# Performance work log

Hardware: AMD Instinct MI355X
Metric: run time of the kernel (lower is better)

The kernel has to match this reference:

```python
import jax, jax.numpy as jnp
import numpy as np

B, H0, W0, C = 8, 56, 56, 256
KC = VC = C
HID = 4 * C
NH = 8  # ChannelAttention default num_heads


def _ln(x, g, b, eps=1e-5):
    m = x.mean(-1, keepdims=True)
    v = jnp.var(x, axis=-1, keepdims=True)
    return (x - m) * jax.lax.rsqrt(v + eps) * g + b


def _dwconv(x, w, b, H, W):
    # x: [B, N, C] -> depthwise 3x3 on [B, C, H, W]
    Bn, N, Cc = x.shape
    t = x.transpose(0, 2, 1).reshape(Bn, Cc, H, W)
    y = jax.lax.conv_general_dilated(t, w, (1, 1), 'SAME', feature_group_count=Cc,
                                     dimension_numbers=('NCHW', 'OIHW', 'NCHW'))
    y = y + b[None, :, None, None]
    return y.reshape(Bn, Cc, H * W).transpose(0, 2, 1)


def _mixffn(x, H, W, w1, b1, dww, dwb, lg, lb, w2, b2):
    f = x @ w1.T + b1  # fc1(x), reused for the skip (torch computes it twice, same value)
    ax = jax.nn.gelu(_ln(_dwconv(f, dww, dwb, H, W) + f, lg, lb), approximate=False)
    return ax @ w2.T + b2


def _eff_attn(xn, kw, kb, qw, qb, vw, vb, rw, rb):
    # 1x1 convs == per-pixel linear; head_count=1
    k = jax.nn.softmax(xn @ kw.T + kb, axis=1)  # softmax over spatial N
    q = jax.nn.softmax(xn @ qw.T + qb, axis=2)  # softmax over key channels
    v = xn @ vw.T + vb
    ctx = jnp.einsum('bnk,bnv->bkv', k, v)      # [B, KC, VC]
    att = jnp.einsum('bkv,bnk->bnv', ctx, q)    # [B, N, VC]
    return att @ rw.T + rb


def _chan_attn(xn, temp, qkv_w, pw, pb):
    Bn, N, Cc = xn.shape
    d = Cc // NH
    qkv = (xn @ qkv_w.T).reshape(Bn, N, 3, NH, d).transpose(2, 0, 3, 4, 1)  # [3,B,h,d,N]
    q, k, v = qkv[0], qkv[1], qkv[2]
    q = q / jnp.maximum(jnp.linalg.norm(q, axis=-1, keepdims=True), 1e-12)
    k = k / jnp.maximum(jnp.linalg.norm(k, axis=-1, keepdims=True), 1e-12)
    attn = jax.nn.softmax(jnp.einsum('bhdn,bhen->bhde', q, k) * temp, axis=-1)  # [B,h,d,d]
    out = jnp.einsum('bhde,bhen->bhdn', attn, v).transpose(0, 3, 1, 2).reshape(Bn, N, Cc)
    return out @ pw.T + pb


def _forward(x, ln1g, ln1b, eakw, eakb, eaqw, eaqb, eavw, eavb, earw, earb,
             ln2g, ln2b, m1w1, m1b1, m1dww, m1dwb, m1lg, m1lb, m1w2, m1b2,
             ln3g, ln3b, catemp, caqkvw, capw, capb,
             ln4g, ln4b, m2w1, m2b1, m2dww, m2dwb, m2lg, m2lb, m2w2, m2b2, H, W):
    add1 = x + _eff_attn(_ln(x, ln1g, ln1b), eakw, eakb, eaqw, eaqb, eavw, eavb, earw, earb)
    add2 = add1 + _mixffn(_ln(add1, ln2g, ln2b), H, W, m1w1, m1b1, m1dww, m1dwb, m1lg, m1lb, m1w2, m1b2)
    add3 = add2 + _chan_attn(_ln(add2, ln3g, ln3b), catemp, caqkvw, capw, capb)
    return add3 + _mixffn(_ln(add3, ln4g, ln4b), H, W, m2w1, m2b1, m2dww, m2dwb, m2lg, m2lb, m2w2, m2b2)


def setup_inputs() -> dict:
    key = jax.random.key(0)
    ks = jax.random.split(key, 16)
    s = 0.02
    rn = lambda k, shape: jax.random.normal(k, shape, jnp.float32) * s
    f32 = jnp.float32
    return {
        'x': jax.random.normal(ks[0], (B, H0 * W0, C), f32),
        'H': H0, 'W': W0,
        'ln1g': jnp.ones(C, f32), 'ln1b': jnp.zeros(C, f32),
        'eakw': rn(ks[1], (KC, C)), 'eakb': jnp.zeros(KC, f32),
        'eaqw': rn(ks[2], (KC, C)), 'eaqb': jnp.zeros(KC, f32),
        'eavw': rn(ks[3], (VC, C)), 'eavb': jnp.zeros(VC, f32),
        'earw': rn(ks[4], (C, VC)), 'earb': jnp.zeros(C, f32),
        'ln2g': jnp.ones(C, f32), 'ln2b': jnp.zeros(C, f32),
        'm1w1': rn(ks[5], (HID, C)), 'm1b1': jnp.zeros(HID, f32),
        'm1dww': rn(ks[6], (HID, 1, 3, 3)), 'm1dwb': jnp.zeros(HID, f32),
        'm1lg': jnp.ones(HID, f32), 'm1lb': jnp.zeros(HID, f32),
        'm1w2': rn(ks[7], (C, HID)), 'm1b2': jnp.zeros(C, f32),
        'ln3g': jnp.ones(C, f32), 'ln3b': jnp.zeros(C, f32),
        'catemp': jnp.ones((NH, 1, 1), f32),
        'caqkvw': rn(ks[8], (3 * C, C)),
        'capw': rn(ks[9], (C, C)), 'capb': jnp.zeros(C, f32),
        'ln4g': jnp.ones(C, f32), 'ln4b': jnp.zeros(C, f32),
        'm2w1': rn(ks[10], (HID, C)), 'm2b1': jnp.zeros(HID, f32),
        'm2dww': rn(ks[11], (HID, 1, 3, 3)), 'm2dwb': jnp.zeros(HID, f32),
        'm2lg': jnp.ones(HID, f32), 'm2lb': jnp.zeros(HID, f32),
        'm2w2': rn(ks[12], (C, HID)), 'm2b2': jnp.zeros(C, f32),
    }


def reference(x, H, W, ln1g, ln1b, eakw, eakb, eaqw, eaqb, eavw, eavb, earw, earb,
              ln2g, ln2b, m1w1, m1b1, m1dww, m1dwb, m1lg, m1lb, m1w2, m1b2,
              ln3g, ln3b, catemp, caqkvw, capw, capb,
              ln4g, ln4b, m2w1, m2b1, m2dww, m2dwb, m2lg, m2lb, m2w2, m2b2):
    return _forward(x, ln1g, ln1b, eakw, eakb, eaqw, eaqb, eavw, eavb, earw, earb,
                    ln2g, ln2b, m1w1, m1b1, m1dww, m1dwb, m1lg, m1lb, m1w2, m1b2,
                    ln3g, ln3b, catemp, caqkvw, capw, capb,
                    ln4g, ln4b, m2w1, m2b1, m2dww, m2dwb, m2lg, m2lb, m2w2, m2b2, H, W)
```

## Files before the change

kernel.cpp:

```cpp
#include <hip/hip_runtime.h>
#include <hip/hip_bf16.h>

typedef __hip_bfloat16 bf16;
typedef __attribute__((ext_vector_type(8))) short short8;
typedef __attribute__((ext_vector_type(4))) float floatx4;

#define DI __device__ __forceinline__

DI unsigned short bfbits(float f){
    bf16 h = __float2bfloat16(f);
    return *reinterpret_cast<unsigned short*>(&h);
}
DI float bu(unsigned short u){
    union { unsigned int i; float f; } x; x.i = ((unsigned int)u) << 16; return x.f;
}

DI float gelu_exact(float x){
    float z = fabsf(x) * 0.70710678118654752f;
    float t = __builtin_amdgcn_rcpf(fmaf(0.3275911f, z, 1.f));
    float p = t * fmaf(t, fmaf(t, fmaf(t, fmaf(t, 1.061405429f, -1.453152027f),
                    1.421413741f), -0.284496736f), 0.254829592f);
    float e = __expf(-z*z);
    float er = fmaf(-p, e, 1.f);
    er = copysignf(er, x);
    return 0.5f * x * (1.f + er);
}

DI void gload16(const void* g, void* l){
    __builtin_amdgcn_global_load_lds(
        (const __attribute__((address_space(1))) unsigned int*)g,
        (__attribute__((address_space(3))) unsigned int*)l,
        16, 0, 0);
}

static constexpr int BATCH = 8;
static constexpr int HH = 56, WW = 56;
static constexpr int NPOS = HH * WW;
static constexpr int CDIM = 256;
static constexpr int HIDD = 1024;
static constexpr int MTOT = BATCH * NPOS;
static constexpr int NCHUNK = 49;
static constexpr int LP = 40;
static constexpr int TNS = 7;

struct WArgs {
    const float* src[10];
    bf16* dst[10];
    int n[10];
};
__global__ __launch_bounds__(256) void wcvt_kernel(WArgs a){
    int wid = blockIdx.y;
    int i = (blockIdx.x*256 + threadIdx.x) * 8;
    if (i >= a.n[wid]) return;
    const float* s = a.src[wid] + i;
    float4 f0 = *(const float4*)(s);
    float4 f1 = *(const float4*)(s + 4);
    union { uint4 u; unsigned short us[8]; } p;
    p.us[0]=bfbits(f0.x); p.us[1]=bfbits(f0.y); p.us[2]=bfbits(f0.z); p.us[3]=bfbits(f0.w);
    p.us[4]=bfbits(f1.x); p.us[5]=bfbits(f1.y); p.us[6]=bfbits(f1.z); p.us[7]=bfbits(f1.w);
    *(uint4*)(a.dst[wid] + i) = p.u;
}

__global__ __launch_bounds__(256) void wtrans_kernel(const float* __restrict__ w1, const float* __restrict__ w2,
                                                     float* __restrict__ t1, float* __restrict__ t2){
    int i = blockIdx.x*256 + threadIdx.x;
    const float* w = blockIdx.y ? w2 : w1;
    float* t = blockIdx.y ? t2 : t1;
    int tap = i >> 10, c = i & 1023;
    t[i] = w[c*9 + tap];
}

template<typename TC>
__global__ __launch_bounds__(256) void mfma_gemm(
    const bf16* __restrict__ A, const bf16* __restrict__ Bw,
    const float* __restrict__ bias, const float* __restrict__ addend,
    TC* __restrict__ C, int M, int N, int K, int lda,
    long long strA, long long strB, long long strC, long long strAdd)
{
    __shared__ __align__(16) float smemf[8192];
    short* S = (short*)smemf;
    int tid = threadIdx.x;
    int bz = blockIdx.z;
    A  += (long long)bz * strA;
    Bw += (long long)bz * strB;
    C  += (long long)bz * strC;
    if (addend) addend += (long long)bz * strAdd;

    int gx = gridDim.x;
    int nwg = gx * gridDim.y;
    int bidl = blockIdx.y * gx + blockIdx.x;
    int qq = nwg >> 3, rr = nwg & 7;
    int xcd = bidl & 7, ixx = bidl >> 3;
    int tile = (xcd < rr) ? (xcd*(qq+1) + ixx) : (rr*(qq+1) + (xcd-rr)*qq + ixx);
    int n0 = (tile % gx) * 128, m0 = (tile / gx) * 128;

    int w = tid >> 6, lane = tid & 63, lm = lane & 15, quad = lane >> 4;
    int mw = (w >> 1) * 64, nw = (w & 1) * 64;

    int c0 = w*128 + lane, c1 = c0 + 64;
    int ar0 = c0 >> 2, ac0 = (c0 & 3) ^ (ar0 & 3);
    int ar1 = c1 >> 2, ac1 = (c1 & 3) ^ (ar1 & 3);
    int rgA0 = m0 + ar0; if (rgA0 > M-1) rgA0 = M-1;
    int rgA1 = m0 + ar1; if (rgA1 > M-1) rgA1 = M-1;
    short* aL0 = S + (2*w+0)*512;
    short* aL1 = S + (2*w+1)*512;
    short* bL0 = S + 4096 + (2*w+0)*512;
    short* bL1 = S + 4096 + (2*w+1)*512;
    const bf16* Arow0 = A + (long long)rgA0*lda + ac0*8;
    const bf16* Arow1 = A + (long long)rgA1*lda + ac1*8;
    const bf16* Brow0 = Bw + (long long)(n0+ar0)*K + ac0*8;
    const bf16* Brow1 = Bw + (long long)(n0+ar1)*K + ac1*8;

    floatx4 z = {0.f, 0.f, 0.f, 0.f};
    floatx4 acc[4][4];
    #pragma unroll
    for (int mi = 0; mi < 4; mi++)
        #pragma unroll
        for (int ni = 0; ni < 4; ni++) acc[mi][ni] = z;

    int sq = quad ^ (lm & 3);

    auto STAGE = [&](int k0, int poff){
        gload16(Arow0 + k0, aL0 + poff);
        gload16(Arow1 + k0, aL1 + poff);
        gload16(Brow0 + k0, bL0 + poff);
        gload16(Brow1 + k0, bL1 + poff);
    };

    STAGE(0, 0);
    __syncthreads();
    int NS = K >> 5;
    for (int st = 0; st < NS; st++){
        int poff = (st & 1) << 13;
        if (st + 1 < NS) STAGE((st+1)*32, poff ^ 8192);
        short8 af[4], bfr[4];
        #pragma unroll
        for (int mi = 0; mi < 4; mi++)
            af[mi] = *(const short8*)&S[poff + (((mw + mi*16 + lm)<<2) + sq)*8];
        #pragma unroll
        for (int ni = 0; ni < 4; ni++)
            bfr[ni] = *(const short8*)&S[poff + 4096 + (((nw + ni*16 + lm)<<2) + sq)*8];
        #pragma unroll
        for (int mi = 0; mi < 4; mi++)
            #pragma unroll
            for (int ni = 0; ni < 4; ni++)
                acc[mi][ni] = __builtin_amdgcn_mfma_f32_16x16x32_bf16(af[mi], bfr[ni], acc[mi][ni], 0, 0, 0);
        __syncthreads();
    }

    float bvv[4];
    #pragma unroll
    for (int ni = 0; ni < 4; ni++)
        bvv[ni] = bias ? bias[n0 + nw + ni*16 + lm] : 0.f;
    float* esc = smemf + w*1088;
    int rl0 = lane >> 3;
    #pragma unroll
    for (int mi = 0; mi < 4; mi++){
        #pragma unroll
        for (int ni = 0; ni < 4; ni++)
            #pragma unroll
            for (int r = 0; r < 4; r++)
                esc[(quad*4 + r)*68 + ni*16 + lm] = acc[mi][ni][r] + bvv[ni];
        #pragma unroll
        for (int p = 0; p < 2; p++){
            int rloc = p*8 + rl0;
            int rg = m0 + mw + mi*16 + rloc;
            if (rg < M){
                if constexpr (sizeof(TC) == 2){
                    int cl = (lane & 7) * 8;
                    float4 u0 = *(const float4*)&esc[rloc*68 + cl];
                    float4 u1 = *(const float4*)&esc[rloc*68 + cl + 4];
                    if (addend){
                        long long ai = (long long)rg*N + (n0 + nw + cl);
                        float4 a0 = *(const float4*)(addend + ai);
                        float4 a1 = *(const float4*)(addend + ai + 4);
                        u0.x+=a0.x; u0.y+=a0.y; u0.z+=a0.z; u0.w+=a0.w;
                        u1.x+=a1.x; u1.y+=a1.y; u1.z+=a1.z; u1.w+=a1.w;
                    }
                    union { uint4 u; unsigned short us[8]; } pk;
                    pk.us[0]=bfbits(u0.x); pk.us[1]=bfbits(u0.y); pk.us[2]=bfbits(u0.z); pk.us[3]=bfbits(u0.w);
                    pk.us[4]=bfbits(u1.x); pk.us[5]=bfbits(u1.y); pk.us[6]=bfbits(u1.z); pk.us[7]=bfbits(u1.w);
                    *(uint4*)(C + (long long)rg*N + (n0 + nw + cl)) = pk.u;
                } else {
                    int cl4 = (lane & 7) * 4;
                    long long co = (long long)rg*N + (n0 + nw);
                    float4 u0 = *(const float4*)&esc[rloc*68 + cl4];
                    float4 u1 = *(const float4*)&esc[rloc*68 + 32 + cl4];
                    if (addend){
                        float4 a0 = *(const float4*)(addend + co + cl4);
                        float4 a1 = *(const float4*)(addend + co + 32 + cl4);
                        u0.x+=a0.x; u0.y+=a0.y; u0.z+=a0.z; u0.w+=a0.w;
                        u1.x+=a1.x; u1.y+=a1.y; u1.z+=a1.z; u1.w+=a1.w;
                    }
                    *(float4*)(C + co + cl4) = u0;
                    *(float4*)(C + co + 32 + cl4) = u1;
                }
            }
        }
    }
}

__global__ __launch_bounds__(256) void gemm_tn_mfma(const bf16* __restrict__ V, const bf16* __restrict__ Kb,
                                                    float* __restrict__ part){
    __shared__ short As[128*LP];
    __shared__ short Bs[128*LP];
    int tid = threadIdx.x;
    int bz = blockIdx.z;
    int b = bz / TNS, s = bz % TNS;
    const bf16* Vb = V  + (long long)b*NPOS*CDIM;
    const bf16* Kc = Kb + (long long)b*NPOS*CDIM;
    int m0 = blockIdx.y * 128, n0 = blockIdx.x * 128;
    int w = tid >> 6, lane = tid & 63, lm = lane & 15, quad = lane >> 4;
    int mw = (w >> 1) * 64, nw = (w & 1) * 64;

    floatx4 z = {0.f,0.f,0.f,0.f};
    floatx4 acc[4][4];
    #pragma unroll
    for (int mi = 0; mi < 4; mi++)
        #pragma unroll
        for (int ni = 0; ni < 4; ni++) acc[mi][ni] = z;

    int r = tid & 31, cgrp = tid >> 5;

    for (int step = 0; step < 448/32; step++){
        int nb = s*448 + step*32;
        #pragma unroll
        for (int cc = 0; cc < 2; cc++){
            int ch = cgrp*8 + cc*64;
            short8 va = *(const short8*)(Vb + (long long)(nb + r)*CDIM + m0 + ch);
            short8 ka = *(const short8*)(Kc + (long long)(nb + r)*CDIM + n0 + ch);
            #pragma unroll
            for (int i = 0; i < 8; i++){
                As[(ch+i)*LP + r] = va[i];
                Bs[(ch+i)*LP + r] = ka[i];
            }
        }
        __syncthreads();
        short8 af[4], bfr[4];
        #pragma unroll
        for (int mi = 0; mi < 4; mi++)
            af[mi] = *(const short8*)&As[(mw + mi*16 + lm)*LP + quad*8];
        #pragma unroll
        for (int ni = 0; ni < 4; ni++)
            bfr[ni] = *(const short8*)&Bs[(nw + ni*16 + lm)*LP + quad*8];
        #pragma unroll
        for (int mi = 0; mi < 4; mi++)
            #pragma unroll
            for (int ni = 0; ni < 4; ni++)
                acc[mi][ni] = __builtin_amdgcn_mfma_f32_16x16x32_bf16(af[mi], bfr[ni], acc[mi][ni], 0, 0, 0);
        __syncthreads();
    }

    float* pb = part + (long long)bz * CDIM * CDIM;
    #pragma unroll
    for (int ni = 0; ni < 4; ni++){
        int cg = n0 + nw + ni*16 + lm;
        #pragma unroll
        for (int mi = 0; mi < 4; mi++){
            #pragma unroll
            for (int rr = 0; rr < 4; rr++){
                int rg = m0 + mw + mi*16 + quad*4 + rr;
                pb[(long long)rg*CDIM + cg] = acc[mi][ni][rr];
            }
        }
    }
}

__global__ __launch_bounds__(256) void ctx_reduce(const float* __restrict__ part, bf16* __restrict__ ctxb){
    long long idx = (long long)blockIdx.x*256 + threadIdx.x;
    int b = (int)(idx >> 16);
    int rem = (int)(idx & 65535);
    float s = 0.f;
    #pragma unroll
    for (int sp = 0; sp < TNS; sp++)
        s += part[((long long)(b*TNS+sp) << 16) + rem];
    ctxb[idx] = __float2bfloat16(s);
}

DI void st4o(float* p, long long i, float a, float b, float c, float d){
    float4 v = make_float4(a,b,c,d); *(float4*)(p + i) = v;
}
DI void st4o(bf16* p, long long i, float a, float b, float c, float d){
    union { unsigned long long u; unsigned short us[4]; } pk;
    pk.us[0]=bfbits(a); pk.us[1]=bfbits(b); pk.us[2]=bfbits(c); pk.us[3]=bfbits(d);
    *(unsigned long long*)(p + i) = pk.u;
}
template<typename TOUT>
__global__ __launch_bounds__(256) void ln4_kernel(const float* __restrict__ x, const float* __restrict__ g,
                                                  const float* __restrict__ b, TOUT* __restrict__ y){
    int wv = threadIdx.x >> 6, lane = threadIdx.x & 63;
    long long row = (long long)blockIdx.x*4 + wv;
    float4 v = *(const float4*)(x + row*256 + lane*4);
    float s  = v.x + v.y + v.z + v.w;
    float ss = v.x*v.x + v.y*v.y + v.z*v.z + v.w*v.w;
    #pragma unroll
    for (int off = 32; off > 0; off >>= 1){
        s  += __shfl_down(s,  off);
        ss += __shfl_down(ss, off);
    }
    s = __shfl(s, 0); ss = __shfl(ss, 0);
    float mean = s * (1.f/256.f);
    float var  = ss * (1.f/256.f) - mean*mean;
    float inv  = rsqrtf(var + 1e-5f);
    float4 gv = *(const float4*)(g + lane*4);
    float4 bv = *(const float4*)(b + lane*4);
    st4o(y, row*256 + lane*4,
         (v.x-mean)*inv*gv.x + bv.x, (v.y-mean)*inv*gv.y + bv.y,
         (v.z-mean)*inv*gv.z + bv.z, (v.w-mean)*inv*gv.w + bv.w);
}

__global__ __launch_bounds__(256) void colsm_p1(const float* __restrict__ x, float* __restrict__ lmax, float* __restrict__ lsum){
    int b = blockIdx.x / NCHUNK, ch = blockIdx.x % NCHUNK;
    int c = threadIdx.x;
    const float* base = x + ((long long)b*NPOS + ch*64)*512 + c;
    float m = -1e30f;
    for (int r = 0; r < 64; r++) m = fmaxf(m, base[(long long)r*512]);
    float s = 0.f;
    for (int r = 0; r < 64; r++) s += expf(base[(long long)r*512] - m);
    lmax[(long long)blockIdx.x*CDIM + c] = m;
    lsum[(long long)blockIdx.x*CDIM + c] = s;
}
__global__ __launch_bounds__(256) void colsm_p2(const float* __restrict__ lmax, const float* __restrict__ lsum,
                                                float* __restrict__ gmax, float* __restrict__ ginv){
    int b = blockIdx.x; int c = threadIdx.x;
    float g = -1e30f;
    for (int ch = 0; ch < NCHUNK; ch++) g = fmaxf(g, lmax[((long long)b*NCHUNK+ch)*CDIM + c]);
    float s = 0.f;
    for (int ch = 0; ch < NCHUNK; ch++)
        s += lsum[((long long)b*NCHUNK+ch)*CDIM + c] * expf(lmax[((long long)b*NCHUNK+ch)*CDIM + c] - g);
    gmax[b*CDIM + c] = g; ginv[b*CDIM + c] = 1.f / s;
}

__global__ __launch_bounds__(256) void kqsm_kernel(const float* __restrict__ x, const float* __restrict__ bias,
                                                   const float* __restrict__ gmax, const float* __restrict__ ginv,
                                                   bf16* __restrict__ kb, bf16* __restrict__ qb){
    int wv = threadIdx.x >> 6, lane = threadIdx.x & 63;
    long long row = (long long)blockIdx.x*4 + wv;
    int b = blockIdx.x / 784;
    float4 v = *(const float4*)(x + row*512 + 256 + lane*4);
    float4 bb = *(const float4*)(bias + lane*4);
    v.x += bb.x; v.y += bb.y; v.z += bb.z; v.w += bb.w;
    float m = fmaxf(fmaxf(v.x, v.y), fmaxf(v.z, v.w));
    #pragma unroll
    for (int off = 32; off > 0; off >>= 1) m = fmaxf(m, __shfl_down(m, off));
    m = __shfl(m, 0);
    float e0 = expf(v.x - m), e1 = expf(v.y - m), e2 = expf(v.z - m), e3 = expf(v.w - m);
    float s = e0 + e1 + e2 + e3;
    #pragma unroll
    for (int off = 32; off > 0; off >>= 1) s += __shfl_down(s, off);
    s = __shfl(s, 0);
    float inv = 1.f / s;
    st4o(qb, row*256 + lane*4, e0*inv, e1*inv, e2*inv, e3*inv);
    float4 kv = *(const float4*)(x + row*512 + lane*4);
    float4 gm = *(const float4*)(gmax + b*CDIM + lane*4);
    float4 gi = *(const float4*)(ginv + b*CDIM + lane*4);
    st4o(kb, row*256 + lane*4,
         expf(kv.x - gm.x)*gi.x, expf(kv.y - gm.y)*gi.y,
         expf(kv.z - gm.z)*gi.z, expf(kv.w - gm.w)*gi.w);
}

template<bool G>
DI void conv_core(const bf16* __restrict__ fb, const float* __restrict__ wT,
                  int h, int pw, int c0, float* acc0, float* acc1){
    #pragma unroll
    for (int r = 0; r < 3; r++){
        int hy = h - 1 + r;
        bool rv = !G || (hy >= 0 && hy < HH);
        int hyc = G ? min(max(hy, 0), HH-1) : hy;
        float u[4][8];
        #pragma unroll
        for (int c = 0; c < 4; c++){
            int wx = pw - 1 + c;
            bool vv = rv && (!G || (wx >= 0 && wx < WW));
            int wxc = G ? min(max(wx, 0), WW-1) : wx;
            uint4 raw = *(const uint4*)(fb + (long long)(hyc*WW + wxc)*HIDD + c0);
            unsigned short* us = (unsigned short*)&raw;
            #pragma unroll
            for (int i = 0; i < 8; i++){
                float xv = bu(us[i]);
                u[c][i] = (G && !vv) ? 0.f : xv;
            }
        }
        #pragma unroll
        for (int kx = 0; kx < 3; kx++){
            float4 wA = *(const float4*)(wT + (r*3+kx)*1024 + c0);
            float4 wB = *(const float4*)(wT + (r*3+kx)*1024 + c0 + 4);
            float wv[8] = {wA.x,wA.y,wA.z,wA.w,wB.x,wB.y,wB.z,wB.w};
            #pragma unroll
            for (int i = 0; i < 8; i++){
                acc0[i] = fmaf(u[kx][i],   wv[i], acc0[i]);
                acc1[i] = fmaf(u[kx+1][i], wv[i], acc1[i]);
            }
        }
        if (r == 1){
            #pragma unroll
            for (int i = 0; i < 8; i++){ acc0[i] += u[1][i]; acc1[i] += u[2][i]; }
        }
    }
}

__global__ __launch_bounds__(256) void dwconv_ln_gelu_kernel(const bf16* __restrict__ f, const float* __restrict__ wT,
        const float* __restrict__ db, const float* __restrict__ lg, const float* __restrict__ lb, bf16* __restrict__ out){
    __shared__ float rs[4][128], rq[4][128], rfin[8];
    int tid = threadIdx.x;
    int b = blockIdx.x & 7;
    int rem = blockIdx.x >> 3;
    int h = rem / 14, w0 = (rem % 14) * 4;
    const bf16* fb = f + (long long)b * NPOS * HIDD;
    int ph = tid >> 7, ct = tid & 127;
    int c0 = ct * 8;
    int pw = w0 + 2*ph;

    float acc0[8], acc1[8];
    {
        float4 d0 = *(const float4*)(db + c0);
        float4 d1 = *(const float4*)(db + c0 + 4);
        acc0[0]=d0.x; acc0[1]=d0.y; acc0[2]=d0.z; acc0[3]=d0.w;
        acc0[4]=d1.x; acc0[5]=d1.y; acc0[6]=d1.z; acc0[7]=d1.w;
        #pragma unroll
        for (int i = 0; i < 8; i++) acc1[i] = acc0[i];
    }
    bool interior = (h > 0) && (h < HH-1) && (w0 > 0) && (w0 < 52);
    if (interior) conv_core<false>(fb, wT, h, pw, c0, acc0, acc1);
    else          conv_core<true >(fb, wT, h, pw, c0, acc0, acc1);

    {
        float s0=0.f, q0=0.f, s1=0.f, q1=0.f;
        #pragma unroll
        for (int i = 0; i < 8; i++){
            s0 += acc0[i]; q0 += acc0[i]*acc0[i];
            s1 += acc1[i]; q1 += acc1[i]*acc1[i];
        }
        rs[2*ph][ct] = s0; rq[2*ph][ct] = q0;
        rs[2*ph+1][ct] = s1; rq[2*ph+1][ct] = q1;
    }
    __syncthreads();
    {
        int wv = tid >> 6, ln = tid & 63;
        float s = rs[wv][ln] + rs[wv][ln+64];
        float q = rq[wv][ln] + rq[wv][ln+64];
        #pragma unroll
        for (int off = 32; off > 0; off >>= 1){
            s += __shfl_down(s, off);
            q += __shfl_down(q, off);
        }
        if (ln == 0){ rfin[wv] = s; rfin[4+wv] = q; }
    }
    __syncthreads();
    float4 g0 = *(const float4*)(lg + c0), g1 = *(const float4*)(lg + c0 + 4);
    float4 b0 = *(const float4*)(lb + c0), b1 = *(const float4*)(lb + c0 + 4);
    float gg[8] = {g0.x,g0.y,g0.z,g0.w,g1.x,g1.y,g1.z,g1.w};
    float bb[8] = {b0.x,b0.y,b0.z,b0.w,b1.x,b1.y,b1.z,b1.w};
    #pragma unroll
    for (int pp = 0; pp < 2; pp++){
        int g = 2*ph + pp;
        long long n = (long long)b*NPOS + h*WW + (pw + pp);
        float mean = rfin[g] * (1.f/HIDD);
        float var  = rfin[4+g] * (1.f/HIDD) - mean*mean;
        float inv  = rsqrtf(var + 1e-5f);
        const float* ac = pp ? acc1 : acc0;
        union { uint4 u; unsigned short us[8]; } ov;
        #pragma unroll
        for (int i = 0; i < 8; i++){
            float o = (ac[i]-mean)*inv*gg[i] + bb[i];
            ov.us[i] = bfbits(gelu_exact(o));
        }
        *(uint4*)(out + n*HIDD + c0) = ov.u;
    }
}

__global__ __launch_bounds__(256) void ssq_p1(const bf16* __restrict__ qkv, float* __restrict__ lss){
    __shared__ float red[4][64][8];
    int b = blockIdx.x / NCHUNK, ch = blockIdx.x % NCHUNK;
    int tid = threadIdx.x;
    int col = (tid & 63) * 8;
    int rg = tid >> 6;
    float s[8] = {0,0,0,0,0,0,0,0};
    for (int r = rg*16; r < rg*16 + 16; r++){
        long long row = (long long)(b*NPOS + ch*64 + r);
        union { uint4 u; unsigned short us[8]; } v;
        v.u = *(const uint4*)(qkv + row*768 + col);
        #pragma unroll
        for (int i = 0; i < 8; i++){ float f = bu(v.us[i]); s[i] += f*f; }
    }
    #pragma unroll
    for (int i = 0; i < 8; i++) red[rg][tid & 63][i] = s[i];
    __syncthreads();
    if (tid < 64){
        #pragma unroll
        for (int i = 0; i < 8; i++){
            float t = red[0][tid][i] + red[1][tid][i] + red[2][tid][i] + red[3][tid][i];
            lss[(long long)blockIdx.x*512 + tid*8 + i] = t;
        }
    }
}
__global__ __launch_bounds__(256) void ssq_p2(const float* __restrict__ lss, float* __restrict__ invn){
    int b = blockIdx.x; int c = blockIdx.y*256 + threadIdx.x;
    float s = 0.f;
    for (int ch = 0; ch < NCHUNK; ch++) s += lss[((long long)b*NCHUNK+ch)*512 + c];
    invn[b*512 + c] = 1.f / fmaxf(sqrtf(s), 1e-12f);
}

__global__ __launch_bounds__(256) void chanattn_qk_part(const bf16* __restrict__ qkv, const float* __restrict__ invn,
                                                        float* __restrict__ part){
    __shared__ float qs[64][36];
    __shared__ float ks[64][36];
    int bz = blockIdx.x;
    int bh = bz / TNS, s = bz % TNS;
    int b = bh >> 3, hh = bh & 7;
    int tid = threadIdx.x;
    int d = tid >> 3, e0 = (tid & 7) * 4;
    int sr = tid >> 2, sc8 = (tid & 3) * 8;
    float invq[8], invk[8];
    {
        float4 a0 = *(const float4*)(invn + b*512 + hh*32 + sc8);
        float4 a1 = *(const float4*)(invn + b*512 + hh*32 + sc8 + 4);
        float4 b0 = *(const float4*)(invn + b*512 + 256 + hh*32 + sc8);
        float4 b1 = *(const float4*)(invn + b*512 + 256 + hh*32 + sc8 + 4);
        invq[0]=a0.x; invq[1]=a0.y; invq[2]=a0.z; invq[3]=a0.w;
        invq[4]=a1.x; invq[5]=a1.y; invq[6]=a1.z; invq[7]=a1.w;
        invk[0]=b0.x; invk[1]=b0.y; invk[2]=b0.z; invk[3]=b0.w;
        invk[4]=b1.x; invk[5]=b1.y; invk[6]=b1.z; invk[7]=b1.w;
    }
    float acc[4] = {0.f,0.f,0.f,0.f};
    for (int it = 0; it < 7; it++){
        int n0 = s*448 + it*64;
        {
            long long rowb = (long long)(b*NPOS + n0 + sr) * 768;
            union { uint4 u; unsigned short us[8]; } qv, kv;
            qv.u = *(const uint4*)(qkv + rowb + hh*32 + sc8);
            kv.u = *(const uint4*)(qkv + rowb + 256 + hh*32 + sc8);
            #pragma unroll
            for (int i = 0; i < 8; i++){
                qs[sr][sc8+i] = bu(qv.us[i]) * invq[i];
                ks[sr][sc8+i] = bu(kv.us[i]) * invk[i];
            }
        }
        __syncthreads();
        #pragma unroll 4
        for (int r = 0; r < 64; r++){
            float qv = qs[r][d];
            #pragma unroll
            for (int j = 0; j < 4; j++) acc[j] += qv * ks[r][e0+j];
        }
        __syncthreads();
    }
    #pragma unroll
    for (int j = 0; j < 4; j++)
        part[(long long)bz*1024 + d*32 + e0 + j] = acc[j];
}
__global__ __launch_bounds__(256) void chanattn_qk_fin(const float* __restrict__ part, const float* __restrict__ temp,
                                                       float* __restrict__ attn){
    __shared__ float att_s[32][33];
    int bh = blockIdx.x;
    int hh = bh & 7;
    int tid = threadIdx.x;
    int d = tid >> 3, e0 = (tid & 7) * 4;
    float t = temp[hh];
    #pragma unroll
    for (int j = 0; j < 4; j++){
        float s = 0.f;
        for (int sp = 0; sp < TNS; sp++)
            s += part[((long long)bh*TNS + sp)*1024 + d*32 + e0 + j];
        att_s[d][e0+j] = s * t;
    }
    __syncthreads();
    if (tid < 32){
        float m = -1e30f;
        for (int e = 0; e < 32; e++) m = fmaxf(m, att_s[tid][e]);
        float s = 0.f;
        for (int e = 0; e < 32; e++){ float ev = expf(att_s[tid][e] - m); att_s[tid][e] = ev; s += ev; }
        float inv = 1.f / s;
        for (int e = 0; e < 32; e++) att_s[tid][e] *= inv;
    }
    __syncthreads();
    #pragma unroll
    for (int j = 0; j < 4; j++)
        attn[(long long)bh*1024 + d*32 + e0 + j] = att_s[d][e0+j];
}

__global__ __launch_bounds__(256) void wcomb_kernel(const float* __restrict__ capw, const float* __restrict__ attn,
                                                    bf16* __restrict__ Wb){
    __shared__ float at_s[8192];
    int b = blockIdx.x, og = blockIdx.y;
    int tid = threadIdx.x;
    #pragma unroll
    for (int j = 0; j < 8; j++)
        *(float4*)&at_s[tid*32 + j*4] = *(const float4*)(attn + (long long)b*8192 + tid*32 + j*4);
    __syncthreads();
    int o = og*32 + (tid & 31);
    int h = tid >> 5;
    float acc[32];
    #pragma unroll
    for (int e = 0; e < 32; e++) acc[e] = 0.f;
    for (int d = 0; d < 32; d++){
        float w = capw[(long long)o*256 + h*32 + d];
        const float* ar = &at_s[h*1024 + d*32];
        #pragma unroll
        for (int eq = 0; eq < 8; eq++){
            float4 av = *(const float4*)(ar + eq*4);
            acc[eq*4+0] += w*av.x; acc[eq*4+1] += w*av.y;
            acc[eq*4+2] += w*av.z; acc[eq*4+3] += w*av.w;
        }
    }
    bf16* dst = Wb + (long long)b*65536 + (long long)o*256 + h*32;
    #pragma unroll
    for (int eq = 0; eq < 4; eq++){
        union { uint4 u; unsigned short us[8]; } p;
        #pragma unroll
        for (int i = 0; i < 8; i++) p.us[i] = bfbits(acc[eq*8+i]);
        *(uint4*)(dst + eq*8) = p.u;
    }
}

extern "C" void kernel_launch(void* const* d_in, const int* in_sizes, int n_in,
                              void* d_out, int out_size, void* d_ws, size_t ws_size,
                              hipStream_t stream){
    const float* x     = (const float*)d_in[0];
    const float* ln1g  = (const float*)d_in[3];
    const float* ln1b  = (const float*)d_in[4];
    const float* eakw  = (const float*)d_in[5];
    const float* eaqw  = (const float*)d_in[7];
    const float* eaqb  = (const float*)d_in[8];
    const float* eavw  = (const float*)d_in[9];
    const float* eavb  = (const float*)d_in[10];
    const float* earw  = (const float*)d_in[11];
    const float* earb  = (const float*)d_in[12];
    const float* ln2g  = (const float*)d_in[13];
    const float* ln2b  = (const float*)d_in[14];
    const float* m1w1  = (const float*)d_in[15];
    const float* m1b1  = (const float*)d_in[16];
    const float* m1dww = (const float*)d_in[17];
    const float* m1dwb = (const float*)d_in[18];
    const float* m1lg  = (const float*)d_in[19];
    const float* m1lb  = (const float*)d_in[20];
    const float* m1w2  = (const float*)d_in[21];
    const float* m1b2  = (const float*)d_in[22];
    const float* ln3g  = (const float*)d_in[23];
    const float* ln3b  = (const float*)d_in[24];
    const float* catemp= (const float*)d_in[25];
    const float* caqkvw= (const float*)d_in[26];
    const float* capw  = (const float*)d_in[27];
    const float* capb  = (const float*)d_in[28];
    const float* ln4g  = (const float*)d_in[29];
    const float* ln4b  = (const float*)d_in[30];
    const float* m2w1  = (const float*)d_in[31];
    const float* m2b1  = (const float*)d_in[32];
    const float* m2dww = (const float*)d_in[33];
    const float* m2dwb = (const float*)d_in[34];
    const float* m2lg  = (const float*)d_in[35];
    const float* m2lb  = (const float*)d_in[36];
    const float* m2w2  = (const float*)d_in[37];
    const float* m2b2  = (const float*)d_in[38];

    char* base = (char*)d_ws;
    auto alloc = [&](size_t nbytes){ char* p = base; base += (nbytes + 255) & ~(size_t)255; return p; };
    constexpr size_t SZ = (size_t)MTOT*CDIM*4;
    float* R  = (float*)alloc(SZ);
    float* A0 = (float*)alloc(SZ);
    float* A1 = (float*)alloc(SZ);
    float* B0 = (float*)alloc(SZ);
    float* B1 = (float*)alloc(SZ);
    bf16* A0b  = (bf16*)A0;
    bf16* kb   = (bf16*)A0;
    bf16* qb   = A0b + (size_t)MTOT*CDIM;
    bf16* vb   = (bf16*)A1;
    float* KQ  = B0;
    bf16* attb = (bf16*)B0;
    bf16* l2b  = (bf16*)A1;
    bf16* F    = (bf16*)B0;
    bf16* G    = (bf16*)A0;
    bf16* l3b  = (bf16*)B0;
    bf16* Qb   = (bf16*)A0;
    bf16* l4b  = (bf16*)A0;
    bf16* ctxb = (bf16*)alloc((size_t)BATCH*CDIM*CDIM*2);
    float* lmax = (float*)alloc((size_t)BATCH*NCHUNK*CDIM*4);
    float* lsum = (float*)alloc((size_t)BATCH*NCHUNK*CDIM*4);
    float* gmax = (float*)alloc((size_t)BATCH*CDIM*4);
    float* ginv = (float*)alloc((size_t)BATCH*CDIM*4);
    float* lss  = (float*)alloc((size_t)BATCH*NCHUNK*512*4);
    float* invn = (float*)alloc((size_t)BATCH*512*4);
    float* attnb= (float*)alloc((size_t)BATCH*8*32*32*4);
    float* ptn  = (float*)alloc((size_t)BATCH*TNS*CDIM*CDIM*4);
    float* pqk  = (float*)alloc((size_t)BATCH*8*TNS*1024*4);
    bf16* wbuf  = (bf16*)alloc((size_t)1572864*2);
    float* wT1  = (float*)alloc((size_t)9216*4);
    float* wT2  = (float*)alloc((size_t)9216*4);
    bf16* Wcb   = (bf16*)alloc((size_t)BATCH*CDIM*CDIM*2);

    bf16* kqw_b    = wbuf;
    bf16* eavw_b   = wbuf + 131072;
    bf16* earw_b   = wbuf + 196608;
    bf16* m1w1_b   = wbuf + 262144;
    bf16* m1w2_b   = wbuf + 524288;
    bf16* caqkvw_b = wbuf + 786432;
    bf16* m2w1_b   = wbuf + 1048576;
    bf16* m2w2_b   = wbuf + 1310720;

    dim3 blk(256);
    constexpr int MB = MTOT/128;
    long long sA1 = (long long)NPOS*CDIM;
    long long sB1 = (long long)CDIM*CDIM;

    {
        WArgs wa;
        const float* srcs[10] = {eakw, eaqw, eavw, earw, m1w1, m1w2, caqkvw, m2w1, m2w2, m2w2};
        bf16* dsts[10] = {kqw_b, kqw_b + 65536, eavw_b, earw_b, m1w1_b, m1w2_b, caqkvw_b, m2w1_b, m2w2_b, m2w2_b};
        int ns[10] = {65536, 65536, 65536, 65536, 262144, 262144, 196608, 262144, 262144, 0};
        for (int i = 0; i < 10; i++){ wa.src[i]=srcs[i]; wa.dst[i]=dsts[i]; wa.n[i]=ns[i]; }
        wcvt_kernel<<<dim3(128,10), blk, 0, stream>>>(wa);
        wtrans_kernel<<<dim3(36,2), blk, 0, stream>>>(m1dww, m2dww, wT1, wT2);
    }

    ln4_kernel<bf16><<<MTOT/4, blk, 0, stream>>>(x, ln1g, ln1b, A0b);
    mfma_gemm<float><<<dim3(4,MB,1), blk, 0, stream>>>(A0b, kqw_b, nullptr, nullptr, KQ, MTOT, 512, 256, 256, 0,0,0,0);
    mfma_gemm<bf16><<<dim3(2,MB,1), blk, 0, stream>>>(A0b, eavw_b, eavb, nullptr, vb, MTOT, 256, 256, 256, 0,0,0,0);
    colsm_p1<<<BATCH*NCHUNK, blk, 0, stream>>>(KQ, lmax, lsum);
    colsm_p2<<<BATCH, blk, 0, stream>>>(lmax, lsum, gmax, ginv);
    kqsm_kernel<<<MTOT/4, blk, 0, stream>>>(KQ, eaqb, gmax, ginv, kb, qb);
    gemm_tn_mfma<<<dim3(2,2,BATCH*TNS), blk, 0, stream>>>(vb, kb, ptn);
    ctx_reduce<<<(BATCH*65536)/256, blk, 0, stream>>>(ptn, ctxb);
    mfma_gemm<bf16><<<dim3(2,25,BATCH), blk, 0, stream>>>(qb, ctxb, nullptr, nullptr, attb,
            NPOS, 256, 256, 256, sA1, sB1, sA1, 0);
    mfma_gemm<float><<<dim3(2,MB,1), blk, 0, stream>>>(attb, earw_b, earb, x, R, MTOT, 256, 256, 256, 0,0,0,0);

    ln4_kernel<bf16><<<MTOT/4, blk, 0, stream>>>(R, ln2g, ln2b, l2b);
    mfma_gemm<bf16><<<dim3(8,MB,1), blk, 0, stream>>>(l2b, m1w1_b, m1b1, nullptr, F, MTOT, 1024, 256, 256, 0,0,0,0);
    dwconv_ln_gelu_kernel<<<BATCH*HH*14, blk, 0, stream>>>(F, wT1, m1dwb, m1lg, m1lb, G);
    mfma_gemm<float><<<dim3(2,MB,1), blk, 0, stream>>>(G, m1w2_b, m1b2, R, R, MTOT, 256, 1024, 1024, 0,0,0,0);

    ln4_kernel<bf16><<<MTOT/4, blk, 0, stream>>>(R, ln3g, ln3b, l3b);
    mfma_gemm<bf16><<<dim3(6,MB,1), blk, 0, stream>>>(l3b, caqkvw_b, nullptr, nullptr, Qb, MTOT, 768, 256, 256, 0,0,0,0);
    ssq_p1<<<BATCH*NCHUNK, blk, 0, stream>>>(Qb, lss);
    ssq_p2<<<dim3(BATCH,2), blk, 0, stream>>>(lss, invn);
    chanattn_qk_part<<<BATCH*8*TNS, blk, 0, stream>>>(Qb, invn, pqk);
    chanattn_qk_fin<<<BATCH*8, blk, 0, stream>>>(pqk, catemp, attnb);
    wcomb_kernel<<<dim3(BATCH,8), blk, 0, stream>>>(capw, attnb, Wcb);
    mfma_gemm<float><<<dim3(2,25,BATCH), blk, 0, stream>>>(Qb + 512, Wcb, capb, R, R,
            NPOS, 256, 256, 768, (long long)NPOS*768, sB1, sA1, sA1);

    ln4_kernel<bf16><<<MTOT/4, blk, 0, stream>>>(R, ln4g, ln4b, l4b);
    mfma_gemm<bf16><<<dim3(8,MB,1), blk, 0, stream>>>(l4b, m2w1_b, m2b1, nullptr, F, MTOT, 1024, 256, 256, 0,0,0,0);
    dwconv_ln_gelu_kernel<<<BATCH*HH*14, blk, 0, stream>>>(F, wT2, m2dwb, m2lg, m2lb, G);
    mfma_gemm<float><<<dim3(2,MB,1), blk, 0, stream>>>(G, m2w2_b, m2b2, R, (float*)d_out, MTOT, 256, 1024, 1024, 0,0,0,0);
}
```

Before: 551.5 us.

## Fuse residual GEMM with following LayerNorm and widen dwconv to 4 pixels per thread

Adds a gemm_ln kernel that computes a 64-row by full-256-column GEMM tile with bias and residual add, then performs the row LayerNorm in the epilogue and emits the bf16 normalized output. This replaces three separate ln4 kernel launches and their reread of the fp32 residual. The depthwise conv kernel now computes four adjacent pixels per thread to reuse loaded input columns, halving the block count. The trade-offs are fewer, larger GEMM blocks with lower parallelism, and higher register usage in the conv.

```diff
diff --git a/kernel.cpp b/kernel.cpp
--- a/kernel.cpp
+++ b/kernel.cpp
@@ -200,6 +200,173 @@
     }
 }
 
+__global__ __launch_bounds__(256) void gemm_ln(
+    const bf16* __restrict__ A, const bf16* __restrict__ Bw,
+    const float* __restrict__ bias, const float* __restrict__ addend,
+    float* __restrict__ C, bf16* __restrict__ lnout,
+    const float* __restrict__ lg, const float* __restrict__ lb,
+    int M, int K, int lda,
+    long long strA, long long strB, long long strC, long long strAdd, long long strLn)
+{
+    __shared__ __align__(16) float smemf[10240];
+    short* S = (short*)smemf;
+    constexpr int POFF = 10240;
+    int tid = threadIdx.x;
+    int bz = blockIdx.z;
+    A      += (long long)bz * strA;
+    Bw     += (long long)bz * strB;
+    C      += (long long)bz * strC;
+    addend += (long long)bz * strAdd;
+    lnout  += (long long)bz * strLn;
+
+    int nwg = gridDim.y;
+    int bidl = blockIdx.y;
+    int qq = nwg >> 3, rr = nwg & 7;
+    int xcd = bidl & 7, ixx = bidl >> 3;
+    int tile = (xcd < rr) ? (xcd*(qq+1) + ixx) : (rr*(qq+1) + (xcd-rr)*qq + ixx);
+    int m0 = tile * 64;
+
+    int w = tid >> 6, lane = tid & 63, lm = lane & 15, quad = lane >> 4;
+    int nw = w * 64;
+
+    const bf16* gp[5];
+    int lo[5];
+    #pragma unroll
+    for (int t5 = 0; t5 < 5; t5++){
+        int t = w*5 + t5;
+        if (t < 4){
+            int c = t*64 + lane;
+            int row = c >> 2, cg = (c & 3) ^ (row & 3);
+            int rg = m0 + row; if (rg > M-1) rg = M-1;
+            gp[t5] = A + (long long)rg*lda + cg*8;
+            lo[t5] = t*512;
+        } else {
+            int c = (t-4)*64 + lane;
+            int row = c >> 2, cg = (c & 3) ^ (row & 3);
+            gp[t5] = Bw + (long long)row*K + cg*8;
+            lo[t5] = 2048 + (t-4)*512;
+        }
+    }
+
+    floatx4 z = {0.f,0.f,0.f,0.f};
+    floatx4 acc[4][4];
+    #pragma unroll
+    for (int mi = 0; mi < 4; mi++)
+        #pragma unroll
+        for (int ni = 0; ni < 4; ni++) acc[mi][ni] = z;
+
+    int sq = quad ^ (lm & 3);
+
+    auto STAGE = [&](int k0, int poff){
+        #pragma unroll
+        for (int t5 = 0; t5 < 5; t5++)
+            gload16(gp[t5] + k0, S + lo[t5] + poff);
+    };
+
+    STAGE(0, 0);
+    __syncthreads();
+    int NS = K >> 5;
+    for (int st = 0; st < NS; st++){
+        int poff = (st & 1) ? POFF : 0;
+        if (st + 1 < NS) STAGE((st+1)*32, poff ^ POFF);
+        short8 af[4], bfr[4];
+        #pragma unroll
+        for (int mi = 0; mi < 4; mi++)
+            af[mi] = *(const short8*)&S[poff + (((mi*16 + lm)<<2) + sq)*8];
+        #pragma unroll
+        for (int ni = 0; ni < 4; ni++)
+            bfr[ni] = *(const short8*)&S[poff + 2048 + (((nw + ni*16 + lm)<<2) + sq)*8];
+        #pragma unroll
+        for (int mi = 0; mi < 4; mi++)
+            #pragma unroll
+            for (int ni = 0; ni < 4; ni++)
+                acc[mi][ni] = __builtin_amdgcn_mfma_f32_16x16x32_bf16(af[mi], bfr[ni], acc[mi][ni], 0, 0, 0);
+        __syncthreads();
+    }
+
+    float bvv[4];
+    #pragma unroll
+    for (int ni = 0; ni < 4; ni++)
+        bvv[ni] = bias[nw + ni*16 + lm];
+    float* esc  = smemf + w*1088;
+    float* ssum = smemf + 4608;
+    float* ssq  = smemf + 4864;
+    float* mrow = smemf + 5120;
+    float* irow = smemf + 5184;
+    int rl0 = lane >> 3, jo = lane & 7;
+    int cl4 = jo * 4;
+    #pragma unroll
+    for (int mi = 0; mi < 4; mi++){
+        #pragma unroll
+        for (int ni = 0; ni < 4; ni++)
+            #pragma unroll
+            for (int r = 0; r < 4; r++)
+                esc[(quad*4 + r)*68 + ni*16 + lm] = acc[mi][ni][r] + bvv[ni];
+        #pragma unroll
+        for (int p = 0; p < 2; p++){
+            int rloc = p*8 + rl0;
+            int rg = m0 + mi*16 + rloc;
+            long long co = (long long)rg*256 + nw;
+            float4 u0 = *(const float4*)&esc[rloc*68 + cl4];
+            float4 u1 = *(const float4*)&esc[rloc*68 + 32 + cl4];
+            float4 a0 = *(const float4*)(addend + co + cl4);
+            float4 a1 = *(const float4*)(addend + co + 32 + cl4);
+            u0.x+=a0.x; u0.y+=a0.y; u0.z+=a0.z; u0.w+=a0.w;
+            u1.x+=a1.x; u1.y+=a1.y; u1.z+=a1.z; u1.w+=a1.w;
+            *(float4*)(C + co + cl4) = u0;
+            *(float4*)(C + co + 32 + cl4) = u1;
+            float s = u0.x+u0.y+u0.z+u0.w + u1.x+u1.y+u1.z+u1.w;
+            float q = u0.x*u0.x+u0.y*u0.y+u0.z*u0.z+u0.w*u0.w
+                    + u1.x*u1.x+u1.y*u1.y+u1.z*u1.z+u1.w*u1.w;
+            #pragma unroll
+            for (int off = 1; off < 8; off <<= 1){
+                s += __shfl_xor(s, off);
+                q += __shfl_xor(q, off);
+            }
+            if (jo == 0){
+                ssum[w*64 + mi*16 + rloc] = s;
+                ssq [w*64 + mi*16 + rloc] = q;
+            }
+        }
+    }
+    __syncthreads();
+    if (tid < 64){
+        float s = ssum[tid] + ssum[64+tid] + ssum[128+tid] + ssum[192+tid];
+        float q = ssq[tid]  + ssq[64+tid]  + ssq[128+tid]  + ssq[192+tid];
+        float mean = s * (1.f/256.f);
+        float var  = q * (1.f/256.f) - mean*mean;
+        mrow[tid] = mean;
+        irow[tid] = rsqrtf(var + 1e-5f);
+    }
+    __syncthreads();
+    int cl8 = jo * 8;
+    float4 gl0 = *(const float4*)(lg + nw + cl8);
+    float4 gl1 = *(const float4*)(lg + nw + cl8 + 4);
+    float4 bl0 = *(const float4*)(lb + nw + cl8);
+    float4 bl1 = *(const float4*)(lb + nw + cl8 + 4);
+    float gg[8] = {gl0.x,gl0.y,gl0.z,gl0.w,gl1.x,gl1.y,gl1.z,gl1.w};
+    float bbv[8] = {bl0.x,bl0.y,bl0.z,bl0.w,bl1.x,bl1.y,bl1.z,bl1.w};
+    #pragma unroll
+    for (int mi = 0; mi < 4; mi++){
+        #pragma unroll
+        for (int p = 0; p < 2; p++){
+            int rloc = p*8 + rl0;
+            int row64 = mi*16 + rloc;
+            int rg = m0 + row64;
+            float mean = mrow[row64], inv = irow[row64];
+            long long co = (long long)rg*256 + nw + cl8;
+            float4 v0 = *(const float4*)(C + co);
+            float4 v1 = *(const float4*)(C + co + 4);
+            float vv[8] = {v0.x,v0.y,v0.z,v0.w,v1.x,v1.y,v1.z,v1.w};
+            union { uint4 u; unsigned short us[8]; } pk;
+            #pragma unroll
+            for (int i = 0; i < 8; i++)
+                pk.us[i] = bfbits((vv[i]-mean)*inv*gg[i] + bbv[i]);
+            *(uint4*)(lnout + co) = pk.u;
+        }
+    }
+}
+
 __global__ __launch_bounds__(256) void gemm_tn_mfma(const bf16* __restrict__ V, const bf16* __restrict__ Kb,
                                                     float* __restrict__ part){
     __shared__ short As[128*LP];
@@ -360,17 +527,17 @@
 }
 
 template<bool G>
-DI void conv_core(const bf16* __restrict__ fb, const float* __restrict__ wT,
-                  int h, int pw, int c0, float* acc0, float* acc1){
+DI void conv_core4(const bf16* __restrict__ fb, const float* __restrict__ wT,
+                   int h, int pw0, int c0, float a[4][8]){
     #pragma unroll
     for (int r = 0; r < 3; r++){
         int hy = h - 1 + r;
         bool rv = !G || (hy >= 0 && hy < HH);
         int hyc = G ? min(max(hy, 0), HH-1) : hy;
-        float u[4][8];
-        #pragma unroll
-        for (int c = 0; c < 4; c++){
-            int wx = pw - 1 + c;
+        float u[6][8];
+        #pragma unroll
+        for (int c = 0; c < 6; c++){
+            int wx = pw0 - 1 + c;
             bool vv = rv && (!G || (wx >= 0 && wx < WW));
             int wxc = G ? min(max(wx, 0), WW-1) : wx;
             uint4 raw = *(const uint4*)(fb + (long long)(hyc*WW + wxc)*HIDD + c0);
@@ -387,64 +554,64 @@
             float4 wB = *(const float4*)(wT + (r*3+kx)*1024 + c0 + 4);
             float wv[8] = {wA.x,wA.y,wA.z,wA.w,wB.x,wB.y,wB.z,wB.w};
             #pragma unroll
-            for (int i = 0; i < 8; i++){
-                acc0[i] = fmaf(u[kx][i],   wv[i], acc0[i]);
-                acc1[i] = fmaf(u[kx+1][i], wv[i], acc1[i]);
-            }
+            for (int j = 0; j < 4; j++)
+                #pragma unroll
+                for (int i = 0; i < 8; i++)
+                    a[j][i] = fmaf(u[kx+j][i], wv[i], a[j][i]);
         }
         if (r == 1){
             #pragma unroll
-            for (int i = 0; i < 8; i++){ acc0[i] += u[1][i]; acc1[i] += u[2][i]; }
+            for (int j = 0; j < 4; j++)
+                #pragma unroll
+                for (int i = 0; i < 8; i++) a[j][i] += u[j+1][i];
         }
     }
 }
 
 __global__ __launch_bounds__(256) void dwconv_ln_gelu_kernel(const bf16* __restrict__ f, const float* __restrict__ wT,
         const float* __restrict__ db, const float* __restrict__ lg, const float* __restrict__ lb, bf16* __restrict__ out){
-    __shared__ float rs[4][128], rq[4][128], rfin[8];
+    __shared__ float rs[8][128], rq[8][128], rfin[16];
     int tid = threadIdx.x;
     int b = blockIdx.x & 7;
     int rem = blockIdx.x >> 3;
-    int h = rem / 14, w0 = (rem % 14) * 4;
+    int h = rem / 7, w0 = (rem % 7) * 8;
     const bf16* fb = f + (long long)b * NPOS * HIDD;
     int ph = tid >> 7, ct = tid & 127;
     int c0 = ct * 8;
-    int pw = w0 + 2*ph;
-
-    float acc0[8], acc1[8];
+    int pw0 = w0 + ph*4;
+
+    float acc[4][8];
     {
         float4 d0 = *(const float4*)(db + c0);
         float4 d1 = *(const float4*)(db + c0 + 4);
-        acc0[0]=d0.x; acc0[1]=d0.y; acc0[2]=d0.z; acc0[3]=d0.w;
-        acc0[4]=d1.x; acc0[5]=d1.y; acc0[6]=d1.z; acc0[7]=d1.w;
-        #pragma unroll
-        for (int i = 0; i < 8; i++) acc1[i] = acc0[i];
-    }
-    bool interior = (h > 0) && (h < HH-1) && (w0 > 0) && (w0 < 52);
-    if (interior) conv_core<false>(fb, wT, h, pw, c0, acc0, acc1);
-    else          conv_core<true >(fb, wT, h, pw, c0, acc0, acc1);
-
-    {
-        float s0=0.f, q0=0.f, s1=0.f, q1=0.f;
-        #pragma unroll
-        for (int i = 0; i < 8; i++){
-            s0 += acc0[i]; q0 += acc0[i]*acc0[i];
-            s1 += acc1[i]; q1 += acc1[i]*acc1[i];
-        }
-        rs[2*ph][ct] = s0; rq[2*ph][ct] = q0;
-        rs[2*ph+1][ct] = s1; rq[2*ph+1][ct] = q1;
+        #pragma unroll
+        for (int j = 0; j < 4; j++){
+            acc[j][0]=d0.x; acc[j][1]=d0.y; acc[j][2]=d0.z; acc[j][3]=d0.w;
+            acc[j][4]=d1.x; acc[j][5]=d1.y; acc[j][6]=d1.z; acc[j][7]=d1.w;
+        }
+    }
+    bool interior = (h >= 1) && (h <= 54) && (pw0 >= 1) && (pw0 <= 51);
+    if (interior) conv_core4<false>(fb, wT, h, pw0, c0, acc);
+    else          conv_core4<true >(fb, wT, h, pw0, c0, acc);
+
+    #pragma unroll
+    for (int j = 0; j < 4; j++){
+        float s = 0.f, q = 0.f;
+        #pragma unroll
+        for (int i = 0; i < 8; i++){ s += acc[j][i]; q += acc[j][i]*acc[j][i]; }
+        rs[ph*4+j][ct] = s; rq[ph*4+j][ct] = q;
     }
     __syncthreads();
     {
-        int wv = tid >> 6, ln = tid & 63;
-        float s = rs[wv][ln] + rs[wv][ln+64];
-        float q = rq[wv][ln] + rq[wv][ln+64];
-        #pragma unroll
-        for (int off = 32; off > 0; off >>= 1){
-            s += __shfl_down(s, off);
-            q += __shfl_down(q, off);
-        }
-        if (ln == 0){ rfin[wv] = s; rfin[4+wv] = q; }
+        int g = tid >> 5, jn = tid & 31;
+        float s = rs[g][jn] + rs[g][jn+32] + rs[g][jn+64] + rs[g][jn+96];
+        float q = rq[g][jn] + rq[g][jn+32] + rq[g][jn+64] + rq[g][jn+96];
+        #pragma unroll
+        for (int off = 16; off > 0; off >>= 1){
+            s += __shfl_xor(s, off);
+            q += __shfl_xor(q, off);
+        }
+        if (jn == 0){ rfin[g] = s; rfin[8+g] = q; }
     }
     __syncthreads();
     float4 g0 = *(const float4*)(lg + c0), g1 = *(const float4*)(lg + c0 + 4);
@@ -452,17 +619,16 @@
     float gg[8] = {g0.x,g0.y,g0.z,g0.w,g1.x,g1.y,g1.z,g1.w};
     float bb[8] = {b0.x,b0.y,b0.z,b0.w,b1.x,b1.y,b1.z,b1.w};
     #pragma unroll
-    for (int pp = 0; pp < 2; pp++){
-        int g = 2*ph + pp;
-        long long n = (long long)b*NPOS + h*WW + (pw + pp);
+    for (int j = 0; j < 4; j++){
+        int g = ph*4 + j;
+        long long n = (long long)b*NPOS + h*WW + (pw0 + j);
         float mean = rfin[g] * (1.f/HIDD);
-        float var  = rfin[4+g] * (1.f/HIDD) - mean*mean;
+        float var  = rfin[8+g] * (1.f/HIDD) - mean*mean;
         float inv  = rsqrtf(var + 1e-5f);
-        const float* ac = pp ? acc1 : acc0;
         union { uint4 u; unsigned short us[8]; } ov;
         #pragma unroll
         for (int i = 0; i < 8; i++){
-            float o = (ac[i]-mean)*inv*gg[i] + bb[i];
+            float o = (acc[j][i]-mean)*inv*gg[i] + bb[i];
             ov.us[i] = bfbits(gelu_exact(o));
         }
         *(uint4*)(out + n*HIDD + c0) = ov.u;
@@ -672,7 +838,6 @@
     bf16* G    = (bf16*)A0;
     bf16* l3b  = (bf16*)B0;
     bf16* Qb   = (bf16*)A0;
-    bf16* l4b  = (bf16*)A0;
     bf16* ctxb = (bf16*)alloc((size_t)BATCH*CDIM*CDIM*2);
     float* lmax = (float*)alloc((size_t)BATCH*NCHUNK*CDIM*4);
     float* lsum = (float*)alloc((size_t)BATCH*NCHUNK*CDIM*4);
@@ -687,6 +852,7 @@
     float* wT1  = (float*)alloc((size_t)9216*4);
     float* wT2  = (float*)alloc((size_t)9216*4);
     bf16* Wcb   = (bf16*)alloc((size_t)BATCH*CDIM*CDIM*2);
+    bf16* l4b   = (bf16*)alloc((size_t)MTOT*CDIM*2);
 
     bf16* kqw_b    = wbuf;
     bf16* eavw_b   = wbuf + 131072;
@@ -699,6 +865,7 @@
 
     dim3 blk(256);
     constexpr int MB = MTOT/128;
+    constexpr int MB64 = MTOT/64;
     long long sA1 = (long long)NPOS*CDIM;
     long long sB1 = (long long)CDIM*CDIM;
 
@@ -722,25 +889,24 @@
     ctx_reduce<<<(BATCH*65536)/256, blk, 0, stream>>>(ptn, ctxb);
     mfma_gemm<bf16><<<dim3(2,25,BATCH), blk, 0, stream>>>(qb, ctxb, nullptr, nullptr, attb,
             NPOS, 256, 256, 256, sA1, sB1, sA1, 0);
-    mfma_gemm<float><<<dim3(2,MB,1), blk, 0, stream>>>(attb, earw_b, earb, x, R, MTOT, 256, 256, 256, 0,0,0,0);
-
-    ln4_kernel<bf16><<<MTOT/4, blk, 0, stream>>>(R, ln2g, ln2b, l2b);
+    gemm_ln<<<dim3(1,MB64,1), blk, 0, stream>>>(attb, earw_b, earb, x, R, l2b, ln2g, ln2b,
+            MTOT, 256, 256, 0,0,0,0,0);
+
     mfma_gemm<bf16><<<dim3(8,MB,1), blk, 0, stream>>>(l2b, m1w1_b, m1b1, nullptr, F, MTOT, 1024, 256, 256, 0,0,0,0);
-    dwconv_ln_gelu_kernel<<<BATCH*HH*14, blk, 0, stream>>>(F, wT1, m1dwb, m1lg, m1lb, G);
-    mfma_gemm<float><<<dim3(2,MB,1), blk, 0, stream>>>(G, m1w2_b, m1b2, R, R, MTOT, 256, 1024, 1024, 0,0,0,0);
-
-    ln4_kernel<bf16><<<MTOT/4, blk, 0, stream>>>(R, ln3g, ln3b, l3b);
+    dwconv_ln_gelu_kernel<<<BATCH*HH*7, blk, 0, stream>>>(F, wT1, m1dwb, m1lg, m1lb, G);
+    gemm_ln<<<dim3(1,MB64,1), blk, 0, stream>>>(G, m1w2_b, m1b2, R, R, l3b, ln3g, ln3b,
+            MTOT, 1024, 1024, 0,0,0,0,0);
+
     mfma_gemm<bf16><<<dim3(6,MB,1), blk, 0, stream>>>(l3b, caqkvw_b, nullptr, nullptr, Qb, MTOT, 768, 256, 256, 0,0,0,0);
     ssq_p1<<<BATCH*NCHUNK, blk, 0, stream>>>(Qb, lss);
     ssq_p2<<<dim3(BATCH,2), blk, 0, stream>>>(lss, invn);
     chanattn_qk_part<<<BATCH*8*TNS, blk, 0, stream>>>(Qb, invn, pqk);
     chanattn_qk_fin<<<BATCH*8, blk, 0, stream>>>(pqk, catemp, attnb);
     wcomb_kernel<<<dim3(BATCH,8), blk, 0, stream>>>(capw, attnb, Wcb);
-    mfma_gemm<float><<<dim3(2,25,BATCH), blk, 0, stream>>>(Qb + 512, Wcb, capb, R, R,
-            NPOS, 256, 256, 768, (long long)NPOS*768, sB1, sA1, sA1);
-
-    ln4_kernel<bf16><<<MTOT/4, blk, 0, stream>>>(R, ln4g, ln4b, l4b);
+    gemm_ln<<<dim3(1,NPOS/64,BATCH), blk, 0, stream>>>(Qb + 512, Wcb, capb, R, R, l4b, ln4g, ln4b,
+            NPOS, 256, 768, (long long)NPOS*768, sB1, sA1, sA1, (long long)NPOS*CDIM);
+
     mfma_gemm<bf16><<<dim3(8,MB,1), blk, 0, stream>>>(l4b, m2w1_b, m2b1, nullptr, F, MTOT, 1024, 256, 256, 0,0,0,0);
-    dwconv_ln_gelu_kernel<<<BATCH*HH*14, blk, 0, stream>>>(F, wT2, m2dwb, m2lg, m2lb, G);
+    dwconv_ln_gelu_kernel<<<BATCH*HH*7, blk, 0, stream>>>(F, wT2, m2dwb, m2lg, m2lb, G);
     mfma_gemm<float><<<dim3(2,MB,1), blk, 0, stream>>>(G, m2w2_b, m2b2, R, (float*)d_out, MTOT, 256, 1024, 1024, 0,0,0,0);
 }
```

Result: faster. 530.5 us (-3.8%).
